# Kernel tuning notes

Hardware: AMD Instinct MI355X
Metric: run time of the kernel (lower is better)

## Reference

```python
import jax, jax.numpy as jnp
import numpy as np

CENTRAL_FRACTION = 0.25
REAL_WEIGHT = 1.0
IMAG_WEIGHT = 1.0
CENTRAL_WEIGHT = 1.0
PERIPHERY_WEIGHT = 1.0


def setup_inputs() -> dict:
    key = jax.random.key(0)
    k1, k2 = jax.random.split(key)
    shape = (32, 2, 640, 640)
    pred = jax.random.normal(k1, shape, dtype=jnp.float32)
    target = jax.random.normal(k2, shape, dtype=jnp.float32)
    return {"pred": pred, "target": target}


def _channel_loss(pred_c, target_c, start, end):
    # pred_c, target_c: [B, H, W]
    # Per-row MSE over central cols averaged over B*H rows == global mean over
    # the central block (same count per row). Likewise MAE over periphery.
    diff = pred_c - target_c
    central = diff[:, :, start:end]
    periphery = jnp.concatenate([diff[:, :, :start], diff[:, :, end:]], axis=-1)
    central_loss = jnp.mean(central * central)
    periphery_loss = jnp.mean(jnp.abs(periphery))
    return CENTRAL_WEIGHT * central_loss + PERIPHERY_WEIGHT * periphery_loss


def reference(pred, target):
    W = pred.shape[-1]
    central_width = int(W * CENTRAL_FRACTION)
    start = (W - central_width) // 2
    end = start + central_width
    real_loss = _channel_loss(pred[:, 0], target[:, 0], start, end)
    imag_loss = _channel_loss(pred[:, 1], target[:, 1], start, end)
    return REAL_WEIGHT * real_loss + IMAG_WEIGHT * imag_loss
```

## Files before the change

### kernel.cpp

```cpp
#include <hip/hip_runtime.h>


#define NBLOCKS 1280
#define NTHREADS 256
#define NTHREADS_TOTAL (NBLOCKS * NTHREADS)
#define ITERS 20

__global__ __launch_bounds__(NTHREADS) void
partial_kernel(const float4* __restrict__ p4,
               const float4* __restrict__ t4,
               float2* __restrict__ partials) {
    int tid = blockIdx.x * NTHREADS + threadIdx.x;

    int w4 = tid % 160;
    bool central = (w4 >= 60) && (w4 < 100);

    float acc_sq = 0.0f;
    float acc_abs = 0.0f;

    #pragma unroll 4
    for (int k = 0; k < ITERS; ++k) {
        int i = tid + k * NTHREADS_TOTAL;
        float4 p = p4[i];
        float4 t = t4[i];
        float d0 = p.x - t.x;
        float d1 = p.y - t.y;
        float d2 = p.z - t.z;
        float d3 = p.w - t.w;
        float s = d0 * d0 + d1 * d1 + d2 * d2 + d3 * d3;
        float a = fabsf(d0) + fabsf(d1) + fabsf(d2) + fabsf(d3);
        acc_sq  += central ? s : 0.0f;
        acc_abs += central ? 0.0f : a;
    }

    for (int off = 32; off > 0; off >>= 1) {
        acc_sq  += __shfl_down(acc_sq,  off, 64);
        acc_abs += __shfl_down(acc_abs, off, 64);
    }

    __shared__ float s_sq[NTHREADS / 64];
    __shared__ float s_abs[NTHREADS / 64];
    int lane = threadIdx.x & 63;
    int wave = threadIdx.x >> 6;
    if (lane == 0) {
        s_sq[wave] = acc_sq;
        s_abs[wave] = acc_abs;
    }
    __syncthreads();
    if (threadIdx.x == 0) {
        float sq = 0.0f, ab = 0.0f;
        #pragma unroll
        for (int w = 0; w < NTHREADS / 64; ++w) {
            sq += s_sq[w];
            ab += s_abs[w];
        }
        partials[blockIdx.x] = make_float2(sq, ab);
    }
}

__global__ __launch_bounds__(64) void
final_kernel(const float2* __restrict__ partials,
             float* __restrict__ out,
             int nparts) {
    double acc_sq = 0.0;
    double acc_abs = 0.0;
    for (int i = threadIdx.x; i < nparts; i += 64) {
        float2 v = partials[i];
        acc_sq += (double)v.x;
        acc_abs += (double)v.y;
    }
    for (int off = 32; off > 0; off >>= 1) {
        acc_sq  += __shfl_down(acc_sq,  off, 64);
        acc_abs += __shfl_down(acc_abs, off, 64);
    }
    if (threadIdx.x == 0) {
        out[0] = (float)(acc_sq / 3276800.0 + acc_abs / 9830400.0);
    }
}

extern "C" void kernel_launch(void* const* d_in, const int* in_sizes, int n_in,
                              void* d_out, int out_size, void* d_ws, size_t ws_size,
                              hipStream_t stream) {
    const float4* pred = (const float4*)d_in[0];
    const float4* targ = (const float4*)d_in[1];
    float* out = (float*)d_out;
    float2* partials = (float2*)d_ws;

    partial_kernel<<<NBLOCKS, NTHREADS, 0, stream>>>(pred, targ, partials);
    final_kernel<<<1, 64, 0, stream>>>(partials, out, NBLOCKS);
}
```

Baseline: 42.14 us.

## Fuse final reduction into partial kernel via last-block atomic counter

Replaces the separate single-block final reduction kernel with a last-block-done pattern. Each block stores its partials and atomically bumps a counter, and the block that finishes last sums all partials in double precision and writes the output. This removes one kernel launch and its dependency gap, but adds a memset launch to reset the counter, plus an atomic and a fence in every block.

```diff
diff --git a/kernel.cpp b/kernel.cpp
--- a/kernel.cpp
+++ b/kernel.cpp
@@ -3,13 +3,15 @@
 
 #define NBLOCKS 1280
 #define NTHREADS 256
-#define NTHREADS_TOTAL (NBLOCKS * NTHREADS)
+#define NTOTAL (NBLOCKS * NTHREADS)
 #define ITERS 20
 
 __global__ __launch_bounds__(NTHREADS) void
-partial_kernel(const float4* __restrict__ p4,
-               const float4* __restrict__ t4,
-               float2* __restrict__ partials) {
+fused_kernel(const float4* __restrict__ p4,
+             const float4* __restrict__ t4,
+             unsigned int* __restrict__ counter,
+             float2* __restrict__ partials,
+             float* __restrict__ out) {
     int tid = blockIdx.x * NTHREADS + threadIdx.x;
 
     int w4 = tid % 160;
@@ -20,7 +22,7 @@
 
     #pragma unroll 4
     for (int k = 0; k < ITERS; ++k) {
-        int i = tid + k * NTHREADS_TOTAL;
+        int i = tid + k * NTOTAL;
         float4 p = p4[i];
         float4 t = t4[i];
         float d0 = p.x - t.x;
@@ -40,6 +42,7 @@
 
     __shared__ float s_sq[NTHREADS / 64];
     __shared__ float s_abs[NTHREADS / 64];
+    __shared__ int amLast;
     int lane = threadIdx.x & 63;
     int wave = threadIdx.x >> 6;
     if (lane == 0) {
@@ -47,34 +50,48 @@
         s_abs[wave] = acc_abs;
     }
     __syncthreads();
+
     if (threadIdx.x == 0) {
-        float sq = 0.0f, ab = 0.0f;
-        #pragma unroll
-        for (int w = 0; w < NTHREADS / 64; ++w) {
-            sq += s_sq[w];
-            ab += s_abs[w];
+        float sq = s_sq[0] + s_sq[1] + s_sq[2] + s_sq[3];
+        float ab = s_abs[0] + s_abs[1] + s_abs[2] + s_abs[3];
+        __hip_atomic_store(&partials[blockIdx.x].x, sq,
+                           __ATOMIC_RELAXED, __HIP_MEMORY_SCOPE_AGENT);
+        __hip_atomic_store(&partials[blockIdx.x].y, ab,
+                           __ATOMIC_RELAXED, __HIP_MEMORY_SCOPE_AGENT);
+        __threadfence();
+        unsigned int prev = __hip_atomic_fetch_add(counter, 1u,
+                                                   __ATOMIC_ACQ_REL,
+                                                   __HIP_MEMORY_SCOPE_AGENT);
+        amLast = (prev == NBLOCKS - 1) ? 1 : 0;
+    }
+    __syncthreads();
+
+    if (amLast) {
+        double dsq = 0.0, dab = 0.0;
+        for (int i = threadIdx.x; i < NBLOCKS; i += NTHREADS) {
+            float x = __hip_atomic_load(&partials[i].x,
+                                        __ATOMIC_RELAXED, __HIP_MEMORY_SCOPE_AGENT);
+            float y = __hip_atomic_load(&partials[i].y,
+                                        __ATOMIC_RELAXED, __HIP_MEMORY_SCOPE_AGENT);
+            dsq += (double)x;
+            dab += (double)y;
         }
-        partials[blockIdx.x] = make_float2(sq, ab);
-    }
-}
-
-__global__ __launch_bounds__(64) void
-final_kernel(const float2* __restrict__ partials,
-             float* __restrict__ out,
-             int nparts) {
-    double acc_sq = 0.0;
-    double acc_abs = 0.0;
-    for (int i = threadIdx.x; i < nparts; i += 64) {
-        float2 v = partials[i];
-        acc_sq += (double)v.x;
-        acc_abs += (double)v.y;
-    }
-    for (int off = 32; off > 0; off >>= 1) {
-        acc_sq  += __shfl_down(acc_sq,  off, 64);
-        acc_abs += __shfl_down(acc_abs, off, 64);
-    }
-    if (threadIdx.x == 0) {
-        out[0] = (float)(acc_sq / 3276800.0 + acc_abs / 9830400.0);
+        for (int off = 32; off > 0; off >>= 1) {
+            dsq += __shfl_down(dsq, off, 64);
+            dab += __shfl_down(dab, off, 64);
+        }
+        __shared__ double d_sq[NTHREADS / 64];
+        __shared__ double d_ab[NTHREADS / 64];
+        if (lane == 0) {
+            d_sq[wave] = dsq;
+            d_ab[wave] = dab;
+        }
+        __syncthreads();
+        if (threadIdx.x == 0) {
+            double fsq = d_sq[0] + d_sq[1] + d_sq[2] + d_sq[3];
+            double fab = d_ab[0] + d_ab[1] + d_ab[2] + d_ab[3];
+            out[0] = (float)(fsq / 3276800.0 + fab / 9830400.0);
+        }
     }
 }
 
@@ -84,8 +101,11 @@
     const float4* pred = (const float4*)d_in[0];
     const float4* targ = (const float4*)d_in[1];
     float* out = (float*)d_out;
-    float2* partials = (float2*)d_ws;
 
-    partial_kernel<<<NBLOCKS, NTHREADS, 0, stream>>>(pred, targ, partials);
-    final_kernel<<<1, 64, 0, stream>>>(partials, out, NBLOCKS);
+    unsigned int* counter = (unsigned int*)d_ws;
+    float2* partials = (float2*)((char*)d_ws + 256);
+
+    hipMemsetAsync(d_ws, 0, 4, stream);
+    fused_kernel<<<NBLOCKS, NTHREADS, 0, stream>>>(pred, targ, counter,
+                                                   partials, out);
 }
```

New measurement: 116.4 us. 2.76x slower.
